# Optimization experiments

Hardware: AMD Instinct MI355X
Metric: run time of the kernel (lower is better)

The kernel has to match this reference:

```python
import jax, jax.numpy as jnp
import numpy as np

B, T, D_MODEL = 2, 2048, 1024
N_HEAD, D_HEAD = 16, 64
EPS = 1e-5


def setup_inputs() -> dict:
    key = jax.random.key(0)
    ks = jax.random.split(key, 6)
    s = 0.02  # init scale
    x = jax.random.normal(ks[0], (B, T, D_MODEL), jnp.float32)
    Wq = jax.random.normal(ks[1], (D_MODEL, N_HEAD * D_HEAD), jnp.float32) * s
    Wk = jax.random.normal(ks[2], (D_MODEL, N_HEAD * D_HEAD), jnp.float32) * s
    Wv = jax.random.normal(ks[3], (D_MODEL, N_HEAD * D_HEAD), jnp.float32) * s
    Wo = jax.random.normal(ks[4], (N_HEAD * D_HEAD, D_MODEL), jnp.float32) * s
    bo = jnp.zeros((D_MODEL,), jnp.float32)
    gamma = jnp.ones((D_MODEL,), jnp.float32)
    beta = jnp.zeros((D_MODEL,), jnp.float32)
    # causal mask: True = masked out (matches masked_fill semantics)
    mask = jnp.triu(jnp.ones((T, T), dtype=bool), k=1)[None, None]  # [1,1,T,T]
    return {"x": x, "Wq": Wq, "Wk": Wk, "Wv": Wv, "Wo": Wo, "bo": bo,
            "gamma": gamma, "beta": beta, "mask": mask}


def reference(x, Wq, Wk, Wv, Wo, bo, gamma, beta, mask):
    B_, T_, D = x.shape
    # pre-LayerNorm (biased variance, eps=1e-5, matching torch)
    mu = jnp.mean(x, axis=-1, keepdims=True)
    var = jnp.mean(jnp.square(x - mu), axis=-1, keepdims=True)
    xn = (x - mu) / jnp.sqrt(var + EPS) * gamma + beta
    # QKV projections (no bias)
    q = (xn @ Wq).reshape(B_, T_, N_HEAD, D_HEAD)
    k = (xn @ Wk).reshape(B_, T_, N_HEAD, D_HEAD)
    v = (xn @ Wv).reshape(B_, T_, N_HEAD, D_HEAD)
    scale = 1.0 / (D_HEAD ** 0.5)
    scores = jnp.einsum('bthd,bshd->bhts', q, k) * scale  # [B,H,T,T]
    scores = jnp.where(mask, -jnp.finfo(scores.dtype).max, scores)
    attn = jax.nn.softmax(scores, axis=-1)
    o = jnp.einsum('bhts,bshd->bthd', attn, v).reshape(B_, T_, N_HEAD * D_HEAD)
    out = o @ Wo + bo  # dropout is identity (eval / p=0)
    # pre_layernorm=True: residual uses the NORMALIZED x (faithful to source)
    return xn + out
```

## Files before the change

### kernel.cpp

```cpp
#include <hip/hip_runtime.h>
#include <hip/hip_bf16.h>

typedef unsigned short u16;
typedef __attribute__((ext_vector_type(8))) short bf16x8;
typedef __attribute__((ext_vector_type(4))) float f32x4;

#define T_SEQ 2048
#define DM 1024
#define NH 16
#define DH 64

__device__ __forceinline__ float bf2f(u16 u) {
  return __uint_as_float(((unsigned int)u) << 16);
}
__device__ __forceinline__ u16 f2bf(float f) {
  unsigned int u = __float_as_uint(f);
  u += 0x7fff + ((u >> 16) & 1);
  return (u16)(u >> 16);
}
__device__ __forceinline__ bool in_is_f32(const void* gamma) {
  return ((const u16*)gamma)[0] != 0x3F80;
}

__global__ __launch_bounds__(256) void ln_k(const void* __restrict__ x,
                                            const void* __restrict__ gamma,
                                            const void* __restrict__ beta,
                                            u16* __restrict__ xn,
                                            float2* __restrict__ stats) {
  bool f32 = in_is_f32(gamma);
  int row = blockIdx.x;
  int t = threadIdx.x;
  float v[4];
  if (f32) {
    float4 u = ((const float4*)((const float*)x + (size_t)row * DM))[t];
    v[0] = u.x; v[1] = u.y; v[2] = u.z; v[3] = u.w;
  } else {
    uint2 u = ((const uint2*)((const u16*)x + (size_t)row * DM))[t];
    v[0] = bf2f((u16)(u.x & 0xffff)); v[1] = bf2f((u16)(u.x >> 16));
    v[2] = bf2f((u16)(u.y & 0xffff)); v[3] = bf2f((u16)(u.y >> 16));
  }
  float s = v[0] + v[1] + v[2] + v[3];
  float ss = v[0]*v[0] + v[1]*v[1] + v[2]*v[2] + v[3]*v[3];
  #pragma unroll
  for (int m = 1; m < 64; m <<= 1) {
    s += __shfl_xor(s, m);
    ss += __shfl_xor(ss, m);
  }
  __shared__ float red[8];
  int wid = t >> 6;
  if ((t & 63) == 0) { red[wid] = s; red[4 + wid] = ss; }
  __syncthreads();
  float S = red[0] + red[1] + red[2] + red[3];
  float SS = red[4] + red[5] + red[6] + red[7];
  float mu = S * (1.0f / DM);
  float var = SS * (1.0f / DM) - mu * mu;
  float rstd = rsqrtf(var + 1e-5f);
  if (t == 0) stats[row] = make_float2(mu, rstd);
  float gv[4], bv[4];
  if (f32) {
    float4 ug = ((const float4*)gamma)[t];
    float4 ub = ((const float4*)beta)[t];
    gv[0] = ug.x; gv[1] = ug.y; gv[2] = ug.z; gv[3] = ug.w;
    bv[0] = ub.x; bv[1] = ub.y; bv[2] = ub.z; bv[3] = ub.w;
  } else {
    uint2 ug = ((const uint2*)gamma)[t];
    uint2 ub = ((const uint2*)beta)[t];
    gv[0] = bf2f((u16)(ug.x & 0xffff)); gv[1] = bf2f((u16)(ug.x >> 16));
    gv[2] = bf2f((u16)(ug.y & 0xffff)); gv[3] = bf2f((u16)(ug.y >> 16));
    bv[0] = bf2f((u16)(ub.x & 0xffff)); bv[1] = bf2f((u16)(ub.x >> 16));
    bv[2] = bf2f((u16)(ub.y & 0xffff)); bv[3] = bf2f((u16)(ub.y >> 16));
  }
  u16 o[4];
  #pragma unroll
  for (int i = 0; i < 4; i++) o[i] = f2bf((v[i] - mu) * rstd * gv[i] + bv[i]);
  uint2 w;
  w.x = (unsigned)o[0] | ((unsigned)o[1] << 16);
  w.y = (unsigned)o[2] | ((unsigned)o[3] << 16);
  *(uint2*)&xn[(size_t)row * DM + t * 4] = w;
}

__global__ __launch_bounds__(256) void transp_cvt(const void* __restrict__ W0,
                                                  const void* __restrict__ W1,
                                                  const void* __restrict__ W2,
                                                  u16* __restrict__ out,
                                                  const void* __restrict__ gamma) {
  bool f32 = in_is_f32(gamma);
  int z = blockIdx.z;
  const void* in = (z == 0) ? W0 : (z == 1) ? W1 : W2;
  u16* dst0 = out + (size_t)z * 1024 * 1024;
  __shared__ __align__(16) u16 tile[64][72];
  int c0 = blockIdx.x * 64, r0 = blockIdx.y * 64;
  int t = threadIdx.x;
  int rr = t >> 2, seg = t & 3;
  u16 w[16];
  if (f32) {
    const float4* p = (const float4*)((const float*)in + (size_t)(r0 + rr) * 1024 + c0 + seg * 16);
    float4 q0 = p[0], q1 = p[1], q2 = p[2], q3 = p[3];
    w[0] = f2bf(q0.x);  w[1] = f2bf(q0.y);  w[2] = f2bf(q0.z);  w[3] = f2bf(q0.w);
    w[4] = f2bf(q1.x);  w[5] = f2bf(q1.y);  w[6] = f2bf(q1.z);  w[7] = f2bf(q1.w);
    w[8] = f2bf(q2.x);  w[9] = f2bf(q2.y);  w[10] = f2bf(q2.z); w[11] = f2bf(q2.w);
    w[12] = f2bf(q3.x); w[13] = f2bf(q3.y); w[14] = f2bf(q3.z); w[15] = f2bf(q3.w);
  } else {
    const u16* p = (const u16*)in + (size_t)(r0 + rr) * 1024 + c0 + seg * 16;
    bf16x8 a0 = *(const bf16x8*)p;
    bf16x8 a1 = *(const bf16x8*)(p + 8);
    #pragma unroll
    for (int i = 0; i < 8; i++) { w[i] = (u16)a0[i]; w[8 + i] = (u16)a1[i]; }
  }
  #pragma unroll
  for (int i = 0; i < 16; i++) tile[rr][seg * 16 + i] = w[i];
  __syncthreads();
  u16 vals[16];
  #pragma unroll
  for (int i = 0; i < 16; i++) vals[i] = tile[seg * 16 + i][rr];
  u16* dst = &dst0[(size_t)(c0 + rr) * 1024 + r0 + seg * 16];
  #pragma unroll
  for (int q = 0; q < 4; q++) {
    ushort4 p4;
    p4.x = vals[4 * q]; p4.y = vals[4 * q + 1]; p4.z = vals[4 * q + 2]; p4.w = vals[4 * q + 3];
    *(ushort4*)(dst + 4 * q) = p4;
  }
}

__global__ __launch_bounds__(256) void gemm128(const u16* __restrict__ A,
                                               const u16* __restrict__ BT,
                                               u16* __restrict__ Cq,
                                               u16* __restrict__ vt,
                                               void* __restrict__ Cout,
                                               const void* __restrict__ bo,
                                               const void* __restrict__ x,
                                               const void* __restrict__ gamma,
                                               const void* __restrict__ beta,
                                               const float2* __restrict__ stats,
                                               int mode) {
  __shared__ __align__(16) u16 As[128 * 32];
  __shared__ __align__(16) u16 Bs[128 * 32];
  const int K = 1024;
  int tid = threadIdx.x;
  int lane = tid & 63, wid = tid >> 6;
  int wm = wid >> 1, wn = wid & 1;
  int m0 = blockIdx.x * 128, n0 = blockIdx.y * 128;
  int quad = lane >> 4, lcol = lane & 15;
  bool vmode = (mode == 0) && (n0 >= 2048);

  f32x4 acc[4][4];
  #pragma unroll
  for (int i = 0; i < 4; i++)
    #pragma unroll
    for (int j = 0; j < 4; j++) acc[i][j] = (f32x4){0.f, 0.f, 0.f, 0.f};

  int srow = tid >> 2, scol = (tid & 3) * 8;
  const u16* Ag0 = A + (size_t)(m0 + srow) * K + scol;
  const u16* Ag1 = A + (size_t)(m0 + 64 + srow) * K + scol;
  const u16* Bg0 = BT + (size_t)(n0 + srow) * K + scol;
  const u16* Bg1 = BT + (size_t)(n0 + 64 + srow) * K + scol;

  uint4 pa0 = *(const uint4*)Ag0;
  uint4 pa1 = *(const uint4*)Ag1;
  uint4 pb0 = *(const uint4*)Bg0;
  uint4 pb1 = *(const uint4*)Bg1;

  for (int k0 = 0; k0 < K; k0 += 32) {
    if (k0) __syncthreads();
    *(uint4*)(As + tid * 8) = pa0;
    *(uint4*)(As + 2048 + tid * 8) = pa1;
    *(uint4*)(Bs + tid * 8) = pb0;
    *(uint4*)(Bs + 2048 + tid * 8) = pb1;
    __syncthreads();
    if (k0 + 32 < K) {
      pa0 = *(const uint4*)(Ag0 + k0 + 32);
      pa1 = *(const uint4*)(Ag1 + k0 + 32);
      pb0 = *(const uint4*)(Bg0 + k0 + 32);
      pb1 = *(const uint4*)(Bg1 + k0 + 32);
    }
    bf16x8 af[4], bfr[4];
    #pragma unroll
    for (int i = 0; i < 4; i++)
      af[i] = *(const bf16x8*)&As[(wm * 64 + i * 16 + lcol) * 32 + quad * 8];
    #pragma unroll
    for (int j = 0; j < 4; j++)
      bfr[j] = *(const bf16x8*)&Bs[(wn * 64 + j * 16 + lcol) * 32 + quad * 8];
    if (vmode) {
      #pragma unroll
      for (int i = 0; i < 4; i++)
        #pragma unroll
        for (int j = 0; j < 4; j++)
          acc[i][j] = __builtin_amdgcn_mfma_f32_16x16x32_bf16(af[i], bfr[j], acc[i][j], 0, 0, 0);
    } else {
      #pragma unroll
      for (int i = 0; i < 4; i++)
        #pragma unroll
        for (int j = 0; j < 4; j++)
          acc[i][j] = __builtin_amdgcn_mfma_f32_16x16x32_bf16(bfr[j], af[i], acc[i][j], 0, 0, 0);
    }
  }

  if (mode == 0) {
    if (n0 < 2048) {
      #pragma unroll
      for (int i = 0; i < 4; i++) {
        int m = m0 + wm * 64 + i * 16 + lcol;
        #pragma unroll
        for (int j = 0; j < 4; j++) {
          int nb = n0 + wn * 64 + j * 16 + quad * 4;
          ushort4 p;
          p.x = f2bf(acc[i][j][0]); p.y = f2bf(acc[i][j][1]);
          p.z = f2bf(acc[i][j][2]); p.w = f2bf(acc[i][j][3]);
          *(ushort4*)&Cq[(size_t)m * 2048 + nb] = p;
        }
      }
    } else {
      #pragma unroll
      for (int i = 0; i < 4; i++)
        #pragma unroll
        for (int j = 0; j < 4; j++) {
          int c = n0 - 2048 + wn * 64 + j * 16 + lcol;
          int h = c >> 6, d = c & 63;
          int tb = m0 + wm * 64 + i * 16 + quad * 4;
          int bb = tb >> 11, tt = tb & 2047;
          ushort4 p;
          p.x = f2bf(acc[i][j][0]); p.y = f2bf(acc[i][j][1]);
          p.z = f2bf(acc[i][j][2]); p.w = f2bf(acc[i][j][3]);
          *(ushort4*)&vt[((size_t)(bb * NH + h) * DH + d) * T_SEQ + tt] = p;
        }
    }
  } else {
    bool f32 = in_is_f32(gamma);
    #pragma unroll
    for (int i = 0; i < 4; i++) {
      int m = m0 + wm * 64 + i * 16 + lcol;
      float2 st = stats[m];
      #pragma unroll
      for (int j = 0; j < 4; j++) {
        int nb = n0 + wn * 64 + j * 16 + quad * 4;
        size_t idx = (size_t)m * DM + nb;
        float g4[4], b4[4], bo4[4], x4[4];
        if (f32) {
          float4 g = *(const float4*)((const float*)gamma + nb);
          float4 be = *(const float4*)((const float*)beta + nb);
          float4 bb = *(const float4*)((const float*)bo + nb);
          float4 xv = *(const float4*)((const float*)x + idx);
          g4[0]=g.x; g4[1]=g.y; g4[2]=g.z; g4[3]=g.w;
          b4[0]=be.x; b4[1]=be.y; b4[2]=be.z; b4[3]=be.w;
          bo4[0]=bb.x; bo4[1]=bb.y; bo4[2]=bb.z; bo4[3]=bb.w;
          x4[0]=xv.x; x4[1]=xv.y; x4[2]=xv.z; x4[3]=xv.w;
        } else {
          const u16* gp = (const u16*)gamma + nb;
          const u16* bp = (const u16*)beta + nb;
          const u16* op = (const u16*)bo + nb;
          const u16* xp = (const u16*)x + idx;
          #pragma unroll
          for (int r = 0; r < 4; r++) {
            g4[r] = bf2f(gp[r]); b4[r] = bf2f(bp[r]);
            bo4[r] = bf2f(op[r]); x4[r] = bf2f(xp[r]);
          }
        }
        float o4[4];
        #pragma unroll
        for (int r = 0; r < 4; r++) {
          float xnv = (x4[r] - st.x) * st.y * g4[r] + b4[r];
          o4[r] = acc[i][j][r] + bo4[r] + xnv;
        }
        if (f32) {
          float4 o; o.x = o4[0]; o.y = o4[1]; o.z = o4[2]; o.w = o4[3];
          *(float4*)((float*)Cout + idx) = o;
        } else {
          ushort4 o;
          o.x = f2bf(o4[0]); o.y = f2bf(o4[1]); o.z = f2bf(o4[2]); o.w = f2bf(o4[3]);
          *(ushort4*)((u16*)Cout + idx) = o;
        }
      }
    }
  }
}

__global__ __launch_bounds__(256) void attn(const u16* __restrict__ qk,
                                            const u16* __restrict__ vt,
                                            u16* __restrict__ o) {
  __shared__ __align__(16) u16 Ks[64 * 72];
  __shared__ __align__(16) u16 Vs[64 * 72];
  __shared__ __align__(16) u16 Psm[4][16 * 72];
  int tid = threadIdx.x;
  int lane = tid & 63, wid = tid >> 6;
  int bh = blockIdx.y;
  int b = bh >> 4, h = bh & 15;
  int quad = lane >> 4, lcol = lane & 15;
  int r0 = tid >> 3, seg8 = (tid & 7) * 8;

  const u16* Kbase = qk + (size_t)(b * T_SEQ) * 2048 + 1024 + h * DH;
  const u16* Vbase = vt + (size_t)(b * NH + h) * DH * T_SEQ;

  #pragma unroll
  for (int pi = 0; pi < 2; pi++) {
    int qt = pi ? (int)blockIdx.x : 31 - (int)blockIdx.x;
    int q0 = qt * 64 + wid * 16;
    const u16* qrow = qk + ((size_t)(b * T_SEQ) + q0 + lcol) * 2048 + h * DH + quad * 8;
    bf16x8 qa0 = *(const bf16x8*)(qrow);
    bf16x8 qa1 = *(const bf16x8*)(qrow + 32);

    f32x4 Oacc[4];
    #pragma unroll
    for (int jd = 0; jd < 4; jd++) Oacc[jd] = (f32x4){0.f, 0.f, 0.f, 0.f};
    float lpart[4] = {0.f, 0.f, 0.f, 0.f};
    int ktmax = qt * 64;

    uint4 kp0 = *(const uint4*)(Kbase + (size_t)r0 * 2048 + seg8);
    uint4 kp1 = *(const uint4*)(Kbase + (size_t)(r0 + 32) * 2048 + seg8);
    uint4 vp0 = *(const uint4*)(Vbase + (size_t)r0 * 2048 + seg8);
    uint4 vp1 = *(const uint4*)(Vbase + (size_t)(r0 + 32) * 2048 + seg8);

    for (int kt = 0; kt <= ktmax; kt += 64) {
      __syncthreads();
      *(uint4*)&Ks[r0 * 72 + seg8] = kp0;
      *(uint4*)&Ks[(r0 + 32) * 72 + seg8] = kp1;
      *(uint4*)&Vs[r0 * 72 + seg8] = vp0;
      *(uint4*)&Vs[(r0 + 32) * 72 + seg8] = vp1;
      __syncthreads();
      if (kt < ktmax) {
        int kn = kt + 64;
        kp0 = *(const uint4*)(Kbase + (size_t)(kn + r0) * 2048 + seg8);
        kp1 = *(const uint4*)(Kbase + (size_t)(kn + r0 + 32) * 2048 + seg8);
        vp0 = *(const uint4*)(Vbase + (size_t)r0 * 2048 + kn + seg8);
        vp1 = *(const uint4*)(Vbase + (size_t)(r0 + 32) * 2048 + kn + seg8);
      }
      f32x4 S[4];
      #pragma unroll
      for (int j = 0; j < 4; j++) {
        bf16x8 kb0 = *(const bf16x8*)&Ks[(j * 16 + lcol) * 72 + quad * 8];
        bf16x8 kb1 = *(const bf16x8*)&Ks[(j * 16 + lcol) * 72 + 32 + quad * 8];
        f32x4 s = (f32x4){0.f, 0.f, 0.f, 0.f};
        s = __builtin_amdgcn_mfma_f32_16x16x32_bf16(qa0, kb0, s, 0, 0, 0);
        s = __builtin_amdgcn_mfma_f32_16x16x32_bf16(qa1, kb1, s, 0, 0, 0);
        S[j] = s;
      }
      if (kt < ktmax) {
        #pragma unroll
        for (int r = 0; r < 4; r++) {
          float rs = 0.f;
          #pragma unroll
          for (int j = 0; j < 4; j++) {
            float p = __expf(S[j][r] * 0.125f);
            S[j][r] = p;
            rs += p;
          }
          lpart[r] += rs;
        }
      } else {
        #pragma unroll
        for (int r = 0; r < 4; r++) {
          int qg = q0 + quad * 4 + r;
          float rs = 0.f;
          #pragma unroll
          for (int j = 0; j < 4; j++) {
            int key = kt + j * 16 + lcol;
            float p = (key <= qg) ? __expf(S[j][r] * 0.125f) : 0.f;
            S[j][r] = p;
            rs += p;
          }
          lpart[r] += rs;
        }
      }
      #pragma unroll
      for (int j = 0; j < 4; j++)
        #pragma unroll
        for (int r = 0; r < 4; r++)
          Psm[wid][(quad * 4 + r) * 72 + j * 16 + lcol] = f2bf(S[j][r]);
      #pragma unroll
      for (int s = 0; s < 2; s++) {
        bf16x8 pa = *(const bf16x8*)&Psm[wid][lcol * 72 + s * 32 + quad * 8];
        #pragma unroll
        for (int jd = 0; jd < 4; jd++) {
          bf16x8 vb = *(const bf16x8*)&Vs[(jd * 16 + lcol) * 72 + s * 32 + quad * 8];
          Oacc[jd] = __builtin_amdgcn_mfma_f32_16x16x32_bf16(pa, vb, Oacc[jd], 0, 0, 0);
        }
      }
    }
    #pragma unroll
    for (int r = 0; r < 4; r++) {
      float rs = lpart[r];
      rs += __shfl_xor(rs, 1);
      rs += __shfl_xor(rs, 2);
      rs += __shfl_xor(rs, 4);
      rs += __shfl_xor(rs, 8);
      float inv = 1.0f / rs;
      int qg = q0 + quad * 4 + r;
      size_t rowbase = ((size_t)(b * T_SEQ) + qg) * DM + h * DH;
      #pragma unroll
      for (int jd = 0; jd < 4; jd++)
        o[rowbase + jd * 16 + lcol] = f2bf(Oacc[jd][r] * inv);
    }
  }
}

extern "C" void kernel_launch(void* const* d_in, const int* in_sizes, int n_in,
                              void* d_out, int out_size, void* d_ws, size_t ws_size,
                              hipStream_t stream) {
  (void)in_sizes; (void)n_in; (void)out_size; (void)ws_size;
  const void* x     = d_in[0];
  const void* Wq    = d_in[1];
  const void* Wk    = d_in[2];
  const void* Wv    = d_in[3];
  const void* Wo    = d_in[4];
  const void* bo    = d_in[5];
  const void* gamma = d_in[6];
  const void* beta  = d_in[7];

  u16* ws = (u16*)d_ws;
  u16* xn   = ws;
  u16* qkb  = xn + (size_t)4096 * 1024;
  u16* vt   = qkb + (size_t)4096 * 2048;
  u16* obWT = vt + (size_t)2 * 16 * 64 * 2048;
  float2* stats = (float2*)(obWT + (size_t)4096 * 1024);
  u16* WT  = obWT;
  u16* WoT = xn;

  ln_k<<<4096, 256, 0, stream>>>(x, gamma, beta, xn, stats);

  transp_cvt<<<dim3(16, 16, 3), 256, 0, stream>>>(Wq, Wk, Wv, WT, gamma);

  gemm128<<<dim3(32, 24), 256, 0, stream>>>(xn, WT, qkb, vt, nullptr,
                                            nullptr, nullptr, gamma, nullptr,
                                            nullptr, 0);

  transp_cvt<<<dim3(16, 16, 1), 256, 0, stream>>>(Wo, Wo, Wo, WoT, gamma);

  attn<<<dim3(16, 32), 256, 0, stream>>>(qkb, vt, obWT);

  gemm128<<<dim3(32, 8), 256, 0, stream>>>(obWT, WoT, nullptr, nullptr,
                                           d_out, bo, x, gamma, beta, stats, 1);
}
```

Before: 241.0 us.

## Merge weight transposes, reuse Q buffer for attention output, use 64-row tiles for output GEMM

After: 618.3 us. +156.6%, slower.

```diff
diff --git a/kernel.cpp b/kernel.cpp
--- a/kernel.cpp
+++ b/kernel.cpp
@@ -82,11 +82,12 @@
 __global__ __launch_bounds__(256) void transp_cvt(const void* __restrict__ W0,
                                                   const void* __restrict__ W1,
                                                   const void* __restrict__ W2,
+                                                  const void* __restrict__ W3,
                                                   u16* __restrict__ out,
                                                   const void* __restrict__ gamma) {
   bool f32 = in_is_f32(gamma);
   int z = blockIdx.z;
-  const void* in = (z == 0) ? W0 : (z == 1) ? W1 : W2;
+  const void* in = (z == 0) ? W0 : (z == 1) ? W1 : (z == 2) ? W2 : W3;
   u16* dst0 = out + (size_t)z * 1024 * 1024;
   __shared__ __align__(16) u16 tile[64][72];
   int c0 = blockIdx.x * 64, r0 = blockIdx.y * 64;
@@ -122,101 +123,111 @@
   }
 }
 
-__global__ __launch_bounds__(256) void gemm128(const u16* __restrict__ A,
-                                               const u16* __restrict__ BT,
-                                               u16* __restrict__ Cq,
-                                               u16* __restrict__ vt,
-                                               void* __restrict__ Cout,
-                                               const void* __restrict__ bo,
-                                               const void* __restrict__ x,
-                                               const void* __restrict__ gamma,
-                                               const void* __restrict__ beta,
-                                               const float2* __restrict__ stats,
-                                               int mode) {
-  __shared__ __align__(16) u16 As[128 * 32];
+template<int TM, int LDA>
+__global__ __launch_bounds__(256, 4) void gemm_k(const u16* __restrict__ A,
+                                                 const u16* __restrict__ BT,
+                                                 u16* __restrict__ Cq,
+                                                 u16* __restrict__ vt,
+                                                 void* __restrict__ Cout,
+                                                 const void* __restrict__ bo,
+                                                 const void* __restrict__ x,
+                                                 const void* __restrict__ gamma,
+                                                 const void* __restrict__ beta,
+                                                 const float2* __restrict__ stats,
+                                                 int mode) {
+  constexpr int NI = (TM == 128) ? 4 : 1;
+  constexpr int NJ = (TM == 128) ? 4 : 8;
+  constexpr int ACH = (TM == 128) ? 2 : 1;
+  __shared__ __align__(16) u16 As[TM * 32];
   __shared__ __align__(16) u16 Bs[128 * 32];
   const int K = 1024;
   int tid = threadIdx.x;
   int lane = tid & 63, wid = tid >> 6;
-  int wm = wid >> 1, wn = wid & 1;
-  int m0 = blockIdx.x * 128, n0 = blockIdx.y * 128;
+  int wm = (TM == 128) ? (wid >> 1) : wid;
+  int wn = (TM == 128) ? (wid & 1) : 0;
+  int m0 = blockIdx.x * TM, n0 = blockIdx.y * 128;
   int quad = lane >> 4, lcol = lane & 15;
   bool vmode = (mode == 0) && (n0 >= 2048);
 
-  f32x4 acc[4][4];
-  #pragma unroll
-  for (int i = 0; i < 4; i++)
-    #pragma unroll
-    for (int j = 0; j < 4; j++) acc[i][j] = (f32x4){0.f, 0.f, 0.f, 0.f};
+  f32x4 acc[NI][NJ];
+  #pragma unroll
+  for (int i = 0; i < NI; i++)
+    #pragma unroll
+    for (int j = 0; j < NJ; j++) acc[i][j] = (f32x4){0.f, 0.f, 0.f, 0.f};
 
   int srow = tid >> 2, scol = (tid & 3) * 8;
-  const u16* Ag0 = A + (size_t)(m0 + srow) * K + scol;
-  const u16* Ag1 = A + (size_t)(m0 + 64 + srow) * K + scol;
-  const u16* Bg0 = BT + (size_t)(n0 + srow) * K + scol;
-  const u16* Bg1 = BT + (size_t)(n0 + 64 + srow) * K + scol;
+  const u16* Ag0 = A + (size_t)(m0 + srow) * LDA + scol;
+  const u16* Ag1 = A + (size_t)(m0 + 64 + srow) * LDA + scol;
+  const u16* Bg0 = BT + (size_t)(n0 + srow) * 1024 + scol;
+  const u16* Bg1 = BT + (size_t)(n0 + 64 + srow) * 1024 + scol;
 
   uint4 pa0 = *(const uint4*)Ag0;
-  uint4 pa1 = *(const uint4*)Ag1;
+  uint4 pa1;
+  if (ACH == 2) pa1 = *(const uint4*)Ag1;
   uint4 pb0 = *(const uint4*)Bg0;
   uint4 pb1 = *(const uint4*)Bg1;
 
   for (int k0 = 0; k0 < K; k0 += 32) {
     if (k0) __syncthreads();
     *(uint4*)(As + tid * 8) = pa0;
-    *(uint4*)(As + 2048 + tid * 8) = pa1;
+    if (ACH == 2) *(uint4*)(As + 2048 + tid * 8) = pa1;
     *(uint4*)(Bs + tid * 8) = pb0;
     *(uint4*)(Bs + 2048 + tid * 8) = pb1;
     __syncthreads();
     if (k0 + 32 < K) {
       pa0 = *(const uint4*)(Ag0 + k0 + 32);
-      pa1 = *(const uint4*)(Ag1 + k0 + 32);
+      if (ACH == 2) pa1 = *(const uint4*)(Ag1 + k0 + 32);
       pb0 = *(const uint4*)(Bg0 + k0 + 32);
       pb1 = *(const uint4*)(Bg1 + k0 + 32);
     }
-    bf16x8 af[4], bfr[4];
-    #pragma unroll
-    for (int i = 0; i < 4; i++)
-      af[i] = *(const bf16x8*)&As[(wm * 64 + i * 16 + lcol) * 32 + quad * 8];
-    #pragma unroll
-    for (int j = 0; j < 4; j++)
-      bfr[j] = *(const bf16x8*)&Bs[(wn * 64 + j * 16 + lcol) * 32 + quad * 8];
+    bf16x8 af[NI], bfr[NJ];
+    #pragma unroll
+    for (int i = 0; i < NI; i++) {
+      int row = (TM == 128) ? (wm * 64 + i * 16 + lcol) : (wm * 16 + lcol);
+      af[i] = *(const bf16x8*)&As[row * 32 + quad * 8];
+    }
+    #pragma unroll
+    for (int j = 0; j < NJ; j++) {
+      int col = ((TM == 128) ? wn * 64 : 0) + j * 16 + lcol;
+      bfr[j] = *(const bf16x8*)&Bs[col * 32 + quad * 8];
+    }
     if (vmode) {
       #pragma unroll
-      for (int i = 0; i < 4; i++)
-        #pragma unroll
-        for (int j = 0; j < 4; j++)
+      for (int i = 0; i < NI; i++)
+        #pragma unroll
+        for (int j = 0; j < NJ; j++)
           acc[i][j] = __builtin_amdgcn_mfma_f32_16x16x32_bf16(af[i], bfr[j], acc[i][j], 0, 0, 0);
     } else {
       #pragma unroll
-      for (int i = 0; i < 4; i++)
-        #pragma unroll
-        for (int j = 0; j < 4; j++)
+      for (int i = 0; i < NI; i++)
+        #pragma unroll
+        for (int j = 0; j < NJ; j++)
           acc[i][j] = __builtin_amdgcn_mfma_f32_16x16x32_bf16(bfr[j], af[i], acc[i][j], 0, 0, 0);
     }
   }
 
   if (mode == 0) {
-    if (n0 < 2048) {
-      #pragma unroll
-      for (int i = 0; i < 4; i++) {
-        int m = m0 + wm * 64 + i * 16 + lcol;
-        #pragma unroll
-        for (int j = 0; j < 4; j++) {
-          int nb = n0 + wn * 64 + j * 16 + quad * 4;
+    if (!vmode) {
+      #pragma unroll
+      for (int i = 0; i < NI; i++) {
+        int m = m0 + ((TM == 128) ? wm * 64 + i * 16 : wm * 16) + lcol;
+        #pragma unroll
+        for (int j = 0; j < NJ; j++) {
+          int nb2 = n0 + ((TM == 128) ? wn * 64 : 0) + j * 16 + quad * 4;
           ushort4 p;
           p.x = f2bf(acc[i][j][0]); p.y = f2bf(acc[i][j][1]);
           p.z = f2bf(acc[i][j][2]); p.w = f2bf(acc[i][j][3]);
-          *(ushort4*)&Cq[(size_t)m * 2048 + nb] = p;
+          *(ushort4*)&Cq[(size_t)m * 2048 + nb2] = p;
         }
       }
     } else {
       #pragma unroll
-      for (int i = 0; i < 4; i++)
-        #pragma unroll
-        for (int j = 0; j < 4; j++) {
-          int c = n0 - 2048 + wn * 64 + j * 16 + lcol;
+      for (int i = 0; i < NI; i++)
+        #pragma unroll
+        for (int j = 0; j < NJ; j++) {
+          int c = n0 - 2048 + ((TM == 128) ? wn * 64 : 0) + j * 16 + lcol;
           int h = c >> 6, d = c & 63;
-          int tb = m0 + wm * 64 + i * 16 + quad * 4;
+          int tb = m0 + ((TM == 128) ? wm * 64 + i * 16 : wm * 16) + quad * 4;
           int bb = tb >> 11, tt = tb & 2047;
           ushort4 p;
           p.x = f2bf(acc[i][j][0]); p.y = f2bf(acc[i][j][1]);
@@ -227,27 +238,27 @@
   } else {
     bool f32 = in_is_f32(gamma);
     #pragma unroll
-    for (int i = 0; i < 4; i++) {
-      int m = m0 + wm * 64 + i * 16 + lcol;
+    for (int i = 0; i < NI; i++) {
+      int m = m0 + ((TM == 128) ? wm * 64 + i * 16 : wm * 16) + lcol;
       float2 st = stats[m];
       #pragma unroll
-      for (int j = 0; j < 4; j++) {
-        int nb = n0 + wn * 64 + j * 16 + quad * 4;
-        size_t idx = (size_t)m * DM + nb;
+      for (int j = 0; j < NJ; j++) {
+        int nb2 = n0 + ((TM == 128) ? wn * 64 : 0) + j * 16 + quad * 4;
+        size_t idx = (size_t)m * DM + nb2;
         float g4[4], b4[4], bo4[4], x4[4];
         if (f32) {
-          float4 g = *(const float4*)((const float*)gamma + nb);
-          float4 be = *(const float4*)((const float*)beta + nb);
-          float4 bb = *(const float4*)((const float*)bo + nb);
+          float4 g = *(const float4*)((const float*)gamma + nb2);
+          float4 be = *(const float4*)((const float*)beta + nb2);
+          float4 bb = *(const float4*)((const float*)bo + nb2);
           float4 xv = *(const float4*)((const float*)x + idx);
           g4[0]=g.x; g4[1]=g.y; g4[2]=g.z; g4[3]=g.w;
           b4[0]=be.x; b4[1]=be.y; b4[2]=be.z; b4[3]=be.w;
           bo4[0]=bb.x; bo4[1]=bb.y; bo4[2]=bb.z; bo4[3]=bb.w;
           x4[0]=xv.x; x4[1]=xv.y; x4[2]=xv.z; x4[3]=xv.w;
         } else {
-          const u16* gp = (const u16*)gamma + nb;
-          const u16* bp = (const u16*)beta + nb;
-          const u16* op = (const u16*)bo + nb;
+          const u16* gp = (const u16*)gamma + nb2;
+          const u16* bp = (const u16*)beta + nb2;
+          const u16* op = (const u16*)bo + nb2;
           const u16* xp = (const u16*)x + idx;
           #pragma unroll
           for (int r = 0; r < 4; r++) {
@@ -384,7 +395,7 @@
       rs += __shfl_xor(rs, 8);
       float inv = 1.0f / rs;
       int qg = q0 + quad * 4 + r;
-      size_t rowbase = ((size_t)(b * T_SEQ) + qg) * DM + h * DH;
+      size_t rowbase = ((size_t)(b * T_SEQ) + qg) * 2048 + h * DH;
       #pragma unroll
       for (int jd = 0; jd < 4; jd++)
         o[rowbase + jd * 16 + lcol] = f2bf(Oacc[jd][r] * inv);
@@ -406,26 +417,24 @@
   const void* beta  = d_in[7];
 
   u16* ws = (u16*)d_ws;
-  u16* xn   = ws;
-  u16* qkb  = xn + (size_t)4096 * 1024;
-  u16* vt   = qkb + (size_t)4096 * 2048;
-  u16* obWT = vt + (size_t)2 * 16 * 64 * 2048;
-  float2* stats = (float2*)(obWT + (size_t)4096 * 1024);
-  u16* WT  = obWT;
-  u16* WoT = xn;
+  u16* xn  = ws;
+  u16* qkb = xn + (size_t)4096 * 1024;
+  u16* vt  = qkb + (size_t)4096 * 2048;
+  u16* WT  = vt + (size_t)2 * 16 * 64 * 2048;
+  float2* stats = (float2*)(WT + (size_t)4096 * 1024);
+  u16* WoT = WT + (size_t)3 * 1024 * 1024;
 
   ln_k<<<4096, 256, 0, stream>>>(x, gamma, beta, xn, stats);
 
-  transp_cvt<<<dim3(16, 16, 3), 256, 0, stream>>>(Wq, Wk, Wv, WT, gamma);
-
-  gemm128<<<dim3(32, 24), 256, 0, stream>>>(xn, WT, qkb, vt, nullptr,
-                                            nullptr, nullptr, gamma, nullptr,
-                                            nullptr, 0);
-
-  transp_cvt<<<dim3(16, 16, 1), 256, 0, stream>>>(Wo, Wo, Wo, WoT, gamma);
-
-  attn<<<dim3(16, 32), 256, 0, stream>>>(qkb, vt, obWT);
-
-  gemm128<<<dim3(32, 8), 256, 0, stream>>>(obWT, WoT, nullptr, nullptr,
-                                           d_out, bo, x, gamma, beta, stats, 1);
-}
+  transp_cvt<<<dim3(16, 16, 4), 256, 0, stream>>>(Wq, Wk, Wv, Wo, WT, gamma);
+
+  gemm_k<128, 1024><<<dim3(32, 24), 256, 0, stream>>>(xn, WT, qkb, vt, nullptr,
+                                                      nullptr, nullptr, gamma,
+                                                      nullptr, nullptr, 0);
+
+  attn<<<dim3(16, 32), 256, 0, stream>>>(qkb, vt, qkb);
+
+  gemm_k<64, 2048><<<dim3(64, 8), 256, 0, stream>>>(qkb, WoT, nullptr, nullptr,
+                                                    d_out, bo, x, gamma, beta,
+                                                    stats, 1);
+}
```
